# Optimization experiments

Hardware: AMD Instinct MI355X
Metric: run time of the kernel (lower is better)

## Reference

```python
import jax, jax.numpy as jnp
import numpy as np

HOPS = 3  # matches init kwarg hops=3


def setup_inputs() -> dict:
    key = jax.random.key(0)
    k1, k2, k3, k4 = jax.random.split(key, 4)
    B, N, D, K = 4, 8192, 128, 32
    x = jax.random.normal(k1, (B, N, D), dtype=jnp.float32)
    knn_idx = jax.random.randint(k2, (B, N, K), 0, N)
    # nn.Linear(dim, 3*dim, bias=False): y = x @ W_qkv  (W stored as (D, 3D))
    W_qkv = jax.random.normal(k3, (D, 3 * D), dtype=jnp.float32) / np.sqrt(D)
    # nn.Linear(dim, dim) with bias
    W_out = jax.random.normal(k4, (D, D), dtype=jnp.float32) / np.sqrt(D)
    b_out = jnp.zeros((D,), dtype=jnp.float32)
    return {"x": x, "knn_idx": knn_idx, "W_qkv": W_qkv, "W_out": W_out, "b_out": b_out}


def reference(x, knn_idx, W_qkv, W_out, b_out):
    B, N, D = x.shape
    K = knn_idx.shape[-1]
    qkv = x @ W_qkv                      # [B,N,3D]
    q, kf, vf = jnp.split(qkv, 3, axis=-1)
    b_ids = jnp.arange(B)[:, None, None]  # broadcast with knn_idx -> (B,N,K)
    denom = K + 1e-6

    def diffuse(f):
        # adj @ f: out[knn_idx[b,n,j]] += f[b,n]; duplicates coalesce-sum.
        return jnp.zeros_like(f).at[b_ids, knn_idx].add(f[:, :, None, :]) / denom

    for _ in range(HOPS):
        vf = diffuse(vf)
        kf = diffuse(kf)

    attn = jnp.sum(q * kf, axis=-1, keepdims=True)  # [B,N,1]
    return (attn * vf) @ W_out + b_out
```

## Files before the change

kernel.cpp:

```cpp
#include <hip/hip_runtime.h>
#include <hip/hip_fp16.h>

#define BB     4
#define NN     8192
#define DD     128
#define KNN    32
#define BN     (BB*NN)
#define NK     (NN*KNN)
#define RPB    64
#define RROWS  128
#define RCAP   4608
#define NRANGE (BB*RPB)
#define SCAP   4608
#define BCAP   48

static __device__ __forceinline__ float inv_denom() { return 1.0f / 32.000001f; }

__global__ void compute_bmat(const float* __restrict__ Wqkv,
                             const float* __restrict__ Wout,
                             float* __restrict__ Bmat,
                             int* __restrict__ gcursor) {
    int e = blockIdx.x;
    int j = threadIdx.x;
    if (e == 0) gcursor[j] = 0;
    float acc = 0.f;
    if (j < DD) {
        int c = j;
        #pragma unroll 4
        for (int d = 0; d < DD; ++d)
            acc += Wqkv[c*3*DD + d] * Wqkv[e*3*DD + DD + d];
    } else {
        int o = j - DD;
        #pragma unroll 4
        for (int d = 0; d < DD; ++d)
            acc += Wqkv[e*3*DD + 2*DD + d] * Wout[d*DD + o];
    }
    Bmat[e*2*DD + j] = acc;
}

__global__ __launch_bounds__(256) void cast16_kernel(const float* __restrict__ in,
                                                     __half* __restrict__ out16) {
    int t = blockIdx.x * 256 + threadIdx.x;
    const float4* p = reinterpret_cast<const float4*>(in) + (size_t)t*2;
    float4 a = p[0], b = p[1];
    uint4 w;
    w.x = __builtin_bit_cast(unsigned, __floats2half2_rn(a.x, a.y));
    w.y = __builtin_bit_cast(unsigned, __floats2half2_rn(a.z, a.w));
    w.z = __builtin_bit_cast(unsigned, __floats2half2_rn(b.x, b.y));
    w.w = __builtin_bit_cast(unsigned, __floats2half2_rn(b.z, b.w));
    *(reinterpret_cast<uint4*>(out16) + t) = w;
}

__global__ __launch_bounds__(256) void partition_kernel(
        const int* __restrict__ idx,
        int* __restrict__ staging,
        int* __restrict__ gcursor) {
    __shared__ int bucket[RPB][BCAP];
    __shared__ int bcnt[RPB];
    __shared__ int gbase[RPB];

    int t  = threadIdx.x;
    int bb = blockIdx.x;
    int batch = bb >> 8;
    int c = bb & 255;
    if (t < RPB) bcnt[t] = 0;
    __syncthreads();

    int4 v = reinterpret_cast<const int4*>(idx)[batch*(NK/4) + c*256 + t];
    int nrow = (c*256 + t) >> 3;
    int mm[4] = {v.x, v.y, v.z, v.w};
    #pragma unroll
    for (int j = 0; j < 4; ++j) {
        int m = mm[j];
        int r = m >> 7;
        int p = atomicAdd(&bcnt[r], 1);
        if (p < BCAP) bucket[r][p] = ((m & 127) << 13) | nrow;
    }
    __syncthreads();

    if (t < RPB) {
        int n = min(bcnt[t], BCAP);
        bcnt[t] = n;
        gbase[t] = atomicAdd(&gcursor[batch*RPB + t], n);
    }
    __syncthreads();

    for (int u = t; u < RPB*BCAP; u += 256) {
        int k = u / BCAP, s = u % BCAP;
        if (s < bcnt[k])
            staging[(size_t)(batch*RPB + k)*SCAP + gbase[k] + s] = bucket[k][s];
    }
}

__global__ __launch_bounds__(512) void bin_kernel(
        const int* __restrict__ staging,
        const int* __restrict__ gcursor,
        unsigned short* __restrict__ srcs16,
        int* __restrict__ meta) {
    __shared__ unsigned short binned[RCAP];
    __shared__ int hist[RROWS], pfx[RROWS], cur[RROWS];

    int t  = threadIdx.x;
    int rg = blockIdx.x;
    int cnt = gcursor[rg];
    if (cnt > SCAP) cnt = SCAP;
    const int* sp = staging + (size_t)rg*SCAP;

    if (t < RROWS) { hist[t] = 0; cur[t] = 0; }
    __syncthreads();

    for (int u = t; u < cnt; u += 512)
        atomicAdd(&hist[sp[u] >> 13], 1);
    __syncthreads();

    if (t < 64) {
        int a = hist[2*t], b = hist[2*t+1];
        int s = a + b;
        #pragma unroll
        for (int d = 1; d < 64; d <<= 1) {
            int v = __shfl_up(s, d, 64);
            if (t >= d) s += v;
        }
        int excl = s - (a + b);
        pfx[2*t]   = excl;
        pfx[2*t+1] = excl + a;
    }
    __syncthreads();

    for (int u = t; u < cnt; u += 512) {
        int e = sp[u];
        int ml = e >> 13;
        int p = atomicAdd(&cur[ml], 1);
        binned[pfx[ml] + p] = (unsigned short)(e & 8191);
    }
    __syncthreads();

    int base = rg * RCAP;
    for (int u = t; u < cnt; u += 512) srcs16[base + u] = binned[u];
    if (t < RROWS) {
        int grow = (rg >> 6)*NN + (rg & 63)*RROWS + t;
        meta[grow] = ((base + pfx[t]) << 8) | min(hist[t], 255);
    }
}

__global__ __launch_bounds__(256) void hop_kernel(
        const __half* __restrict__ fin, __half* __restrict__ fout,
        const int* __restrict__ meta,
        const unsigned short* __restrict__ srcs16) {
    int i = blockIdx.x;
    int xcd = i & 7;
    int batch = xcd >> 1;
    int j = ((i >> 3) << 1) | (xcd & 1);
    int wave = threadIdx.x >> 6;
    int lane = threadIdx.x & 63;
    int h = lane >> 4;
    int l16 = lane & 15;
    int g0 = batch*NN + j*8 + wave*2;

    int mt0 = meta[g0], mt1 = meta[g0 + 1];
    int off0 = mt0 >> 8, cnt0 = mt0 & 255;
    int off1 = mt1 >> 8, cnt1 = mt1 & 255;
    const unsigned short* sp0 = srcs16 + off0;
    const unsigned short* sp1 = srcs16 + off1;
    const __half* fbatch = fin + (size_t)batch*NN*DD;
    int laneoff = l16*8;

    int sA[8], sB[8];
    #pragma unroll
    for (int u = 0; u < 8; ++u) {
        int a = sp0[h + 4*u]; sA[u] = (a > NN-1) ? 0 : a;
        int b = sp1[h + 4*u]; sB[u] = (b > NN-1) ? 0 : b;
    }
    uint4 vA[8], vB[8];
    #pragma unroll
    for (int u = 0; u < 8; ++u)
        vA[u] = *reinterpret_cast<const uint4*>(fbatch + (size_t)sA[u]*DD + laneoff);
    #pragma unroll
    for (int u = 0; u < 8; ++u)
        vB[u] = *reinterpret_cast<const uint4*>(fbatch + (size_t)sB[u]*DD + laneoff);

    float acc0[8] = {0,0,0,0,0,0,0,0};
    float acc1[8] = {0,0,0,0,0,0,0,0};
    auto accum = [](float* acc, const uint4& v, float m) {
        float2 f0 = __half22float2(__builtin_bit_cast(__half2, v.x));
        float2 f1 = __half22float2(__builtin_bit_cast(__half2, v.y));
        float2 f2 = __half22float2(__builtin_bit_cast(__half2, v.z));
        float2 f3 = __half22float2(__builtin_bit_cast(__half2, v.w));
        acc[0] = fmaf(f0.x, m, acc[0]); acc[1] = fmaf(f0.y, m, acc[1]);
        acc[2] = fmaf(f1.x, m, acc[2]); acc[3] = fmaf(f1.y, m, acc[3]);
        acc[4] = fmaf(f2.x, m, acc[4]); acc[5] = fmaf(f2.y, m, acc[5]);
        acc[6] = fmaf(f3.x, m, acc[6]); acc[7] = fmaf(f3.y, m, acc[7]);
    };
    #pragma unroll
    for (int u = 0; u < 8; ++u) {
        accum(acc0, vA[u], (h + 4*u < cnt0) ? 1.f : 0.f);
        accum(acc1, vB[u], (h + 4*u < cnt1) ? 1.f : 0.f);
    }

    if (cnt0 > 32) {
        uint4 v2[4]; int s2[4];
        #pragma unroll
        for (int u = 0; u < 4; ++u) {
            int s = sp0[32 + h + 4*u]; s2[u] = (s > NN-1) ? 0 : s;
        }
        #pragma unroll
        for (int u = 0; u < 4; ++u)
            v2[u] = *reinterpret_cast<const uint4*>(fbatch + (size_t)s2[u]*DD + laneoff);
        #pragma unroll
        for (int u = 0; u < 4; ++u)
            accum(acc0, v2[u], (32 + h + 4*u < cnt0) ? 1.f : 0.f);
        for (int e = 48 + h; e < cnt0; e += 4) {
            int s = sp0[e];
            uint4 v = *reinterpret_cast<const uint4*>(fbatch + (size_t)s*DD + laneoff);
            accum(acc0, v, 1.f);
        }
    }
    if (cnt1 > 32) {
        uint4 v2[4]; int s2[4];
        #pragma unroll
        for (int u = 0; u < 4; ++u) {
            int s = sp1[32 + h + 4*u]; s2[u] = (s > NN-1) ? 0 : s;
        }
        #pragma unroll
        for (int u = 0; u < 4; ++u)
            v2[u] = *reinterpret_cast<const uint4*>(fbatch + (size_t)s2[u]*DD + laneoff);
        #pragma unroll
        for (int u = 0; u < 4; ++u)
            accum(acc1, v2[u], (32 + h + 4*u < cnt1) ? 1.f : 0.f);
        for (int e = 48 + h; e < cnt1; e += 4) {
            int s = sp1[e];
            uint4 v = *reinterpret_cast<const uint4*>(fbatch + (size_t)s*DD + laneoff);
            accum(acc1, v, 1.f);
        }
    }

    #pragma unroll
    for (int q = 0; q < 8; ++q) {
        acc0[q] += __shfl_xor(acc0[q], 16);
        acc0[q] += __shfl_xor(acc0[q], 32);
        acc1[q] += __shfl_xor(acc1[q], 16);
        acc1[q] += __shfl_xor(acc1[q], 32);
    }

    const float s = inv_denom();
    if (h == 0) {
        uint4 w;
        w.x = __builtin_bit_cast(unsigned, __floats2half2_rn(acc0[0]*s, acc0[1]*s));
        w.y = __builtin_bit_cast(unsigned, __floats2half2_rn(acc0[2]*s, acc0[3]*s));
        w.z = __builtin_bit_cast(unsigned, __floats2half2_rn(acc0[4]*s, acc0[5]*s));
        w.w = __builtin_bit_cast(unsigned, __floats2half2_rn(acc0[6]*s, acc0[7]*s));
        *reinterpret_cast<uint4*>(fout + (size_t)g0*DD + laneoff) = w;
    } else if (h == 1) {
        uint4 w;
        w.x = __builtin_bit_cast(unsigned, __floats2half2_rn(acc1[0]*s, acc1[1]*s));
        w.y = __builtin_bit_cast(unsigned, __floats2half2_rn(acc1[2]*s, acc1[3]*s));
        w.z = __builtin_bit_cast(unsigned, __floats2half2_rn(acc1[4]*s, acc1[5]*s));
        w.w = __builtin_bit_cast(unsigned, __floats2half2_rn(acc1[6]*s, acc1[7]*s));
        *reinterpret_cast<uint4*>(fout + (size_t)(g0+1)*DD + laneoff) = w;
    }
}

__global__ __launch_bounds__(256) void final_kernel(
        const __half* __restrict__ x3h, const float* __restrict__ x,
        const float* __restrict__ Bmat, const float* __restrict__ bout,
        float* __restrict__ out) {
    __shared__ float a_lds[64][DD];
    int t = threadIdx.x;
    int tc = t & 31, tr = t >> 5;
    int row0 = blockIdx.x * 64;

    for (int u = t; u < 64*16; u += 256) {
        int r = u >> 4, cp = u & 15;
        uint4 v = *reinterpret_cast<const uint4*>(
            x3h + (size_t)(row0 + r)*DD + cp*8);
        float2 f0 = __half22float2(__builtin_bit_cast(__half2, v.x));
        float2 f1 = __half22float2(__builtin_bit_cast(__half2, v.y));
        float2 f2 = __half22float2(__builtin_bit_cast(__half2, v.z));
        float2 f3 = __half22float2(__builtin_bit_cast(__half2, v.w));
        float4* dst = reinterpret_cast<float4*>(&a_lds[r][cp*8]);
        dst[0] = make_float4(f0.x, f0.y, f1.x, f1.y);
        dst[1] = make_float4(f2.x, f2.y, f3.x, f3.y);
    }

    const float* bp0 = Bmat + tc*4;
    const float* bp1 = Bmat + 128 + tc*4;
    float4 pa0[4], pa1[4], pb0[4], pb1[4];
    #pragma unroll
    for (int kk = 0; kk < 4; ++kk) {
        pa0[kk] = *reinterpret_cast<const float4*>(bp0 + kk*256);
        pa1[kk] = *reinterpret_cast<const float4*>(bp1 + kk*256);
    }
    __syncthreads();

    float acc[8][8];
    #pragma unroll
    for (int r = 0; r < 8; ++r)
        #pragma unroll
        for (int u = 0; u < 8; ++u) acc[r][u] = 0.f;

    #pragma unroll 1
    for (int k0 = 0; k0 < DD; k0 += 8) {
        int kn = (k0 + 4 < DD) ? (k0 + 4) : 0;
        #pragma unroll
        for (int kk = 0; kk < 4; ++kk) {
            pb0[kk] = *reinterpret_cast<const float4*>(bp0 + (kn+kk)*256);
            pb1[kk] = *reinterpret_cast<const float4*>(bp1 + (kn+kk)*256);
        }
        {
            float4 av[8];
            #pragma unroll
            for (int r = 0; r < 8; ++r)
                av[r] = *reinterpret_cast<const float4*>(&a_lds[tr*8 + r][k0]);
            #pragma unroll
            for (int kk = 0; kk < 4; ++kk) {
                #pragma unroll
                for (int r = 0; r < 8; ++r) {
                    float a = (kk == 0) ? av[r].x : (kk == 1) ? av[r].y
                            : (kk == 2) ? av[r].z : av[r].w;
                    acc[r][0] += a*pa0[kk].x; acc[r][1] += a*pa0[kk].y;
                    acc[r][2] += a*pa0[kk].z; acc[r][3] += a*pa0[kk].w;
                    acc[r][4] += a*pa1[kk].x; acc[r][5] += a*pa1[kk].y;
                    acc[r][6] += a*pa1[kk].z; acc[r][7] += a*pa1[kk].w;
                }
            }
        }
        int km = (k0 + 8 < DD) ? (k0 + 8) : 0;
        #pragma unroll
        for (int kk = 0; kk < 4; ++kk) {
            pa0[kk] = *reinterpret_cast<const float4*>(bp0 + (km+kk)*256);
            pa1[kk] = *reinterpret_cast<const float4*>(bp1 + (km+kk)*256);
        }
        {
            float4 av[8];
            #pragma unroll
            for (int r = 0; r < 8; ++r)
                av[r] = *reinterpret_cast<const float4*>(&a_lds[tr*8 + r][k0 + 4]);
            #pragma unroll
            for (int kk = 0; kk < 4; ++kk) {
                #pragma unroll
                for (int r = 0; r < 8; ++r) {
                    float a = (kk == 0) ? av[r].x : (kk == 1) ? av[r].y
                            : (kk == 2) ? av[r].z : av[r].w;
                    acc[r][0] += a*pb0[kk].x; acc[r][1] += a*pb0[kk].y;
                    acc[r][2] += a*pb0[kk].z; acc[r][3] += a*pb0[kk].w;
                    acc[r][4] += a*pb1[kk].x; acc[r][5] += a*pb1[kk].y;
                    acc[r][6] += a*pb1[kk].z; acc[r][7] += a*pb1[kk].w;
                }
            }
        }
    }

    float at[8];
    #pragma unroll
    for (int r = 0; r < 8; ++r) {
        int row = row0 + tr*8 + r;
        float4 xv = *reinterpret_cast<const float4*>(x + (size_t)row*DD + tc*4);
        float p = xv.x*acc[r][0] + xv.y*acc[r][1]
                + xv.z*acc[r][2] + xv.w*acc[r][3];
        p += __shfl_xor(p, 1);  p += __shfl_xor(p, 2);
        p += __shfl_xor(p, 4);  p += __shfl_xor(p, 8);
        p += __shfl_xor(p, 16);
        at[r] = p;
    }
    float4 bo = *reinterpret_cast<const float4*>(bout + tc*4);
    #pragma unroll
    for (int r = 0; r < 8; ++r) {
        int row = row0 + tr*8 + r;
        float4 o;
        o.x = at[r]*acc[r][4] + bo.x;
        o.y = at[r]*acc[r][5] + bo.y;
        o.z = at[r]*acc[r][6] + bo.z;
        o.w = at[r]*acc[r][7] + bo.w;
        *reinterpret_cast<float4*>(out + (size_t)row*DD + tc*4) = o;
    }
}

extern "C" void kernel_launch(void* const* d_in, const int* in_sizes, int n_in,
                              void* d_out, int out_size, void* d_ws, size_t ws_size,
                              hipStream_t stream) {
    const float* x    = (const float*)d_in[0];
    const int*   idx  = (const int*)  d_in[1];
    const float* Wqkv = (const float*)d_in[2];
    const float* Wout = (const float*)d_in[3];
    const float* bout = (const float*)d_in[4];
    float* out = (float*)d_out;

    char* ws = (char*)d_ws;
    __half*         x16     = (__half*)(ws);
    __half*         fa16    = (__half*)(ws + 8388608);
    __half*         fb16    = (__half*)(ws + 16777216);
    unsigned short* srcs16  = (unsigned short*)(ws + 25165824);
    int*            meta    = (int*)(ws + 27525376);
    float*          Bmat    = (float*)(ws + 27656448);
    int*            staging = (int*)(ws + 27787520);
    int*            gcursor = (int*)(ws + 32506112);

    compute_bmat<<<DD, 256, 0, stream>>>(Wqkv, Wout, Bmat, gcursor);
    cast16_kernel<<<BN*DD/8/256, 256, 0, stream>>>(x, x16);
    partition_kernel<<<1024, 256, 0, stream>>>(idx, staging, gcursor);
    bin_kernel<<<NRANGE, 512, 0, stream>>>(staging, gcursor, srcs16, meta);

    hop_kernel<<<4096, 256, 0, stream>>>(x16,  fa16, meta, srcs16);
    hop_kernel<<<4096, 256, 0, stream>>>(fa16, fb16, meta, srcs16);
    hop_kernel<<<4096, 256, 0, stream>>>(fb16, fa16, meta, srcs16);

    final_kernel<<<BN/64, 256, 0, stream>>>(fa16, x, Bmat, bout, out);
}
```

Baseline: 125.0 us.

## Use MFMA f16 matrix cores for final projection with transposed fp16 weights

Replaces the scalar FP32 register-tiled GEMM in the final kernel with MFMA 16x16x32 f16 instructions. The combined weight matrix is now stored transposed in fp16 so B fragments can be loaded directly. Waves split into two roles, one computing the attention dot product and one producing the output, and they exchange attention scalars through shared memory. This removes the LDS staging and FP32 FMA cost, at the price of fp16 rounding of the weight matrix and less coalesced scalar stores in the epilogue.

```diff
diff --git a/kernel.cpp b/kernel.cpp
--- a/kernel.cpp
+++ b/kernel.cpp
@@ -14,11 +14,14 @@
 #define SCAP   4608
 #define BCAP   48
 
+typedef _Float16 half8 __attribute__((ext_vector_type(8)));
+typedef float f32x4 __attribute__((ext_vector_type(4)));
+
 static __device__ __forceinline__ float inv_denom() { return 1.0f / 32.000001f; }
 
 __global__ void compute_bmat(const float* __restrict__ Wqkv,
                              const float* __restrict__ Wout,
-                             float* __restrict__ Bmat,
+                             _Float16* __restrict__ BT16,
                              int* __restrict__ gcursor) {
     int e = blockIdx.x;
     int j = threadIdx.x;
@@ -35,7 +38,7 @@
         for (int d = 0; d < DD; ++d)
             acc += Wqkv[e*3*DD + 2*DD + d] * Wout[d*DD + o];
     }
-    Bmat[e*2*DD + j] = acc;
+    BT16[(size_t)j*DD + e] = (_Float16)acc;
 }
 
 __global__ __launch_bounds__(256) void cast16_kernel(const float* __restrict__ in,
@@ -260,118 +263,68 @@
     }
 }
 
-__global__ __launch_bounds__(256) void final_kernel(
+__global__ __launch_bounds__(256) void final_mfma(
         const __half* __restrict__ x3h, const float* __restrict__ x,
-        const float* __restrict__ Bmat, const float* __restrict__ bout,
+        const _Float16* __restrict__ BT16, const float* __restrict__ bout,
         float* __restrict__ out) {
-    __shared__ float a_lds[64][DD];
+    __shared__ float attn_l[2][16];
     int t = threadIdx.x;
-    int tc = t & 31, tr = t >> 5;
-    int row0 = blockIdx.x * 64;
-
-    for (int u = t; u < 64*16; u += 256) {
-        int r = u >> 4, cp = u & 15;
-        uint4 v = *reinterpret_cast<const uint4*>(
-            x3h + (size_t)(row0 + r)*DD + cp*8);
-        float2 f0 = __half22float2(__builtin_bit_cast(__half2, v.x));
-        float2 f1 = __half22float2(__builtin_bit_cast(__half2, v.y));
-        float2 f2 = __half22float2(__builtin_bit_cast(__half2, v.z));
-        float2 f3 = __half22float2(__builtin_bit_cast(__half2, v.w));
-        float4* dst = reinterpret_cast<float4*>(&a_lds[r][cp*8]);
-        dst[0] = make_float4(f0.x, f0.y, f1.x, f1.y);
-        dst[1] = make_float4(f2.x, f2.y, f3.x, f3.y);
-    }
-
-    const float* bp0 = Bmat + tc*4;
-    const float* bp1 = Bmat + 128 + tc*4;
-    float4 pa0[4], pa1[4], pb0[4], pb1[4];
-    #pragma unroll
-    for (int kk = 0; kk < 4; ++kk) {
-        pa0[kk] = *reinterpret_cast<const float4*>(bp0 + kk*256);
-        pa1[kk] = *reinterpret_cast<const float4*>(bp1 + kk*256);
-    }
-    __syncthreads();
-
-    float acc[8][8];
-    #pragma unroll
-    for (int r = 0; r < 8; ++r)
-        #pragma unroll
-        for (int u = 0; u < 8; ++u) acc[r][u] = 0.f;
-
-    #pragma unroll 1
-    for (int k0 = 0; k0 < DD; k0 += 8) {
-        int kn = (k0 + 4 < DD) ? (k0 + 4) : 0;
-        #pragma unroll
-        for (int kk = 0; kk < 4; ++kk) {
-            pb0[kk] = *reinterpret_cast<const float4*>(bp0 + (kn+kk)*256);
-            pb1[kk] = *reinterpret_cast<const float4*>(bp1 + (kn+kk)*256);
-        }
-        {
-            float4 av[8];
+    int w = t >> 6;
+    int lane = t & 63;
+    int role = w & 1;
+    int rh = w >> 1;
+    int row0 = blockIdx.x * 32 + rh * 16;
+    int lr = lane & 15;
+    int lg = lane >> 4;
+
+    const _Float16* x3p = reinterpret_cast<const _Float16*>(x3h);
+
+    half8 a[4];
+    #pragma unroll
+    for (int kc = 0; kc < 4; ++kc)
+        a[kc] = *reinterpret_cast<const half8*>(
+            x3p + (size_t)(row0 + lr)*DD + kc*32 + lg*8);
+
+    f32x4 acc[8];
+    #pragma unroll
+    for (int ti = 0; ti < 8; ++ti) {
+        acc[ti] = (f32x4){0.f, 0.f, 0.f, 0.f};
+        int col = role*128 + ti*16 + lr;
+        const _Float16* bp = BT16 + (size_t)col*DD + lg*8;
+        #pragma unroll
+        for (int kc = 0; kc < 4; ++kc) {
+            half8 b = *reinterpret_cast<const half8*>(bp + kc*32);
+            acc[ti] = __builtin_amdgcn_mfma_f32_16x16x32_f16(a[kc], b, acc[ti], 0, 0, 0);
+        }
+    }
+
+    if (role == 0) {
+        #pragma unroll
+        for (int reg = 0; reg < 4; ++reg) {
+            int row = row0 + lg*4 + reg;
+            const float* xr = x + (size_t)row*DD;
+            float p = 0.f;
             #pragma unroll
-            for (int r = 0; r < 8; ++r)
-                av[r] = *reinterpret_cast<const float4*>(&a_lds[tr*8 + r][k0]);
+            for (int ti = 0; ti < 8; ++ti)
+                p = fmaf(acc[ti][reg], xr[ti*16 + lr], p);
+            p += __shfl_xor(p, 1); p += __shfl_xor(p, 2);
+            p += __shfl_xor(p, 4); p += __shfl_xor(p, 8);
+            if (lr == 0) attn_l[rh][lg*4 + reg] = p;
+        }
+    }
+    __syncthreads();
+    if (role == 1) {
+        #pragma unroll
+        for (int reg = 0; reg < 4; ++reg) {
+            int row = row0 + lg*4 + reg;
+            float at = attn_l[rh][lg*4 + reg];
+            float* orow = out + (size_t)row*DD;
             #pragma unroll
-            for (int kk = 0; kk < 4; ++kk) {
-                #pragma unroll
-                for (int r = 0; r < 8; ++r) {
-                    float a = (kk == 0) ? av[r].x : (kk == 1) ? av[r].y
-                            : (kk == 2) ? av[r].z : av[r].w;
-                    acc[r][0] += a*pa0[kk].x; acc[r][1] += a*pa0[kk].y;
-                    acc[r][2] += a*pa0[kk].z; acc[r][3] += a*pa0[kk].w;
-                    acc[r][4] += a*pa1[kk].x; acc[r][5] += a*pa1[kk].y;
-                    acc[r][6] += a*pa1[kk].z; acc[r][7] += a*pa1[kk].w;
-                }
+            for (int ti = 0; ti < 8; ++ti) {
+                int col = ti*16 + lr;
+                orow[col] = fmaf(at, acc[ti][reg], bout[col]);
             }
         }
-        int km = (k0 + 8 < DD) ? (k0 + 8) : 0;
-        #pragma unroll
-        for (int kk = 0; kk < 4; ++kk) {
-            pa0[kk] = *reinterpret_cast<const float4*>(bp0 + (km+kk)*256);
-            pa1[kk] = *reinterpret_cast<const float4*>(bp1 + (km+kk)*256);
-        }
-        {
-            float4 av[8];
-            #pragma unroll
-            for (int r = 0; r < 8; ++r)
-                av[r] = *reinterpret_cast<const float4*>(&a_lds[tr*8 + r][k0 + 4]);
-            #pragma unroll
-            for (int kk = 0; kk < 4; ++kk) {
-                #pragma unroll
-                for (int r = 0; r < 8; ++r) {
-                    float a = (kk == 0) ? av[r].x : (kk == 1) ? av[r].y
-                            : (kk == 2) ? av[r].z : av[r].w;
-                    acc[r][0] += a*pb0[kk].x; acc[r][1] += a*pb0[kk].y;
-                    acc[r][2] += a*pb0[kk].z; acc[r][3] += a*pb0[kk].w;
-                    acc[r][4] += a*pb1[kk].x; acc[r][5] += a*pb1[kk].y;
-                    acc[r][6] += a*pb1[kk].z; acc[r][7] += a*pb1[kk].w;
-                }
-            }
-        }
-    }
-
-    float at[8];
-    #pragma unroll
-    for (int r = 0; r < 8; ++r) {
-        int row = row0 + tr*8 + r;
-        float4 xv = *reinterpret_cast<const float4*>(x + (size_t)row*DD + tc*4);
-        float p = xv.x*acc[r][0] + xv.y*acc[r][1]
-                + xv.z*acc[r][2] + xv.w*acc[r][3];
-        p += __shfl_xor(p, 1);  p += __shfl_xor(p, 2);
-        p += __shfl_xor(p, 4);  p += __shfl_xor(p, 8);
-        p += __shfl_xor(p, 16);
-        at[r] = p;
-    }
-    float4 bo = *reinterpret_cast<const float4*>(bout + tc*4);
-    #pragma unroll
-    for (int r = 0; r < 8; ++r) {
-        int row = row0 + tr*8 + r;
-        float4 o;
-        o.x = at[r]*acc[r][4] + bo.x;
-        o.y = at[r]*acc[r][5] + bo.y;
-        o.z = at[r]*acc[r][6] + bo.z;
-        o.w = at[r]*acc[r][7] + bo.w;
-        *reinterpret_cast<float4*>(out + (size_t)row*DD + tc*4) = o;
     }
 }
 
@@ -391,11 +344,11 @@
     __half*         fb16    = (__half*)(ws + 16777216);
     unsigned short* srcs16  = (unsigned short*)(ws + 25165824);
     int*            meta    = (int*)(ws + 27525376);
-    float*          Bmat    = (float*)(ws + 27656448);
+    _Float16*       BT16    = (_Float16*)(ws + 27656448);
     int*            staging = (int*)(ws + 27787520);
     int*            gcursor = (int*)(ws + 32506112);
 
-    compute_bmat<<<DD, 256, 0, stream>>>(Wqkv, Wout, Bmat, gcursor);
+    compute_bmat<<<DD, 256, 0, stream>>>(Wqkv, Wout, BT16, gcursor);
     cast16_kernel<<<BN*DD/8/256, 256, 0, stream>>>(x, x16);
     partition_kernel<<<1024, 256, 0, stream>>>(idx, staging, gcursor);
     bin_kernel<<<NRANGE, 512, 0, stream>>>(staging, gcursor, srcs16, meta);
@@ -404,5 +357,5 @@
     hop_kernel<<<4096, 256, 0, stream>>>(fa16, fb16, meta, srcs16);
     hop_kernel<<<4096, 256, 0, stream>>>(fb16, fa16, meta, srcs16);
 
-    final_kernel<<<BN/64, 256, 0, stream>>>(fa16, x, Bmat, bout, out);
-}
+    final_mfma<<<BN/32, 256, 0, stream>>>(fa16, x, BT16, bout, out);
+}
```

Result: faster. 115.7 us (-7.4%).
